# Performance work log

Measured on AMD Instinct MI355X. Metric: run time of the kernel, lower is better.

## Reference

```python
import jax, jax.numpy as jnp
import numpy as np

N_NODES = 50000
N_EDGES = 600000
HIDDEN = 128
HEADS = 8
OUT_CH = HIDDEN // HEADS
NUM_LAYERS = 3
NEG_SLOPE = 0.2   # PyG GATConv default leaky_relu slope
BN_EPS = 1e-5

# Note: dropout is a no-op in eval mode; BatchNorm uses batch statistics
# (training-mode math, the only well-defined choice without running stats).

def setup_inputs() -> dict:
    key = jax.random.key(0)
    ks = jax.random.split(key, 9)
    x = jax.random.normal(ks[0], (N_NODES, HIDDEN), dtype=jnp.float32)
    edge_index = jax.random.randint(ks[1], (2, N_EDGES), 0, N_NODES, dtype=jnp.int64)
    s = 1.0 / np.sqrt(HIDDEN)
    W = jax.random.normal(ks[2], (NUM_LAYERS, HIDDEN, HEADS * OUT_CH), dtype=jnp.float32) * s
    att_src = jax.random.normal(ks[3], (NUM_LAYERS, HEADS, OUT_CH), dtype=jnp.float32) * s
    att_dst = jax.random.normal(ks[4], (NUM_LAYERS, HEADS, OUT_CH), dtype=jnp.float32) * s
    bias = jnp.zeros((NUM_LAYERS, HIDDEN), dtype=jnp.float32)
    gamma = jnp.ones((NUM_LAYERS, HIDDEN), dtype=jnp.float32)
    beta = jnp.zeros((NUM_LAYERS, HIDDEN), dtype=jnp.float32)
    return {"x": x, "edge_index": edge_index, "W": W, "att_src": att_src,
            "att_dst": att_dst, "bias": bias, "gamma": gamma, "beta": beta}


def _gat_layer(x, src, dst, W, a_src, a_dst, b):
    n = x.shape[0]
    h = (x @ W).reshape(n, HEADS, OUT_CH)              # [N,H,C]
    alpha_s = jnp.einsum('nhc,hc->nh', h, a_src)        # [N,H]
    alpha_d = jnp.einsum('nhc,hc->nh', h, a_dst)
    e = jax.nn.leaky_relu(alpha_s[src] + alpha_d[dst], NEG_SLOPE)  # [E,H]
    # segment softmax over incoming edges of each destination node
    m = jax.ops.segment_max(e, dst, num_segments=n)     # [N,H]
    e = jnp.exp(e - m[dst])
    z = jax.ops.segment_sum(e, dst, num_segments=n)
    alpha = e / (z[dst] + 1e-16)                        # [E,H]
    msg = h[src] * alpha[:, :, None]                    # [E,H,C]
    out = jax.ops.segment_sum(msg, dst, num_segments=n) # [N,H,C]
    return out.reshape(n, HEADS * OUT_CH) + b


def _batchnorm(x, gamma, beta):
    mu = x.mean(axis=0)
    var = x.var(axis=0)
    return (x - mu) * jax.lax.rsqrt(var + BN_EPS) * gamma + beta


def reference(x, edge_index, W, att_src, att_dst, bias, gamma, beta):
    src, dst = edge_index[0], edge_index[1]
    for l in range(NUM_LAYERS):
        x = _gat_layer(x, src, dst, W[l], att_src[l], att_dst[l], bias[l])
        x = _batchnorm(x, gamma[l], beta[l])
        x = jax.nn.elu(x)
    return x
```

## Files before the change

### kernel.cpp

```cpp
#include <hip/hip_runtime.h>
#include <hip/hip_bf16.h>

#define N_NODES 50000
#define N_EDGES 600000
#define HID 128
#define HEADS 8
#define OUTC 16
#define NEG_SLOPE 0.2f
#define BN_EPS 1e-5f

typedef __attribute__((ext_vector_type(8))) short short8;
typedef __attribute__((ext_vector_type(4))) float floatx4;

__device__ __forceinline__ float bf_lo(unsigned int v) { return __uint_as_float(v << 16); }
__device__ __forceinline__ float bf_hi(unsigned int v) { return __uint_as_float(v & 0xffff0000u); }

__device__ __forceinline__ short f2bfs(float v) {
    __hip_bfloat16 b = __float2bfloat16(v);
    return *reinterpret_cast<short*>(&b);
}

__global__ void k_hist_prep(const int* __restrict__ dst, int* __restrict__ deg, int e, int nb_e,
                            const float* __restrict__ W, const float* __restrict__ asrc,
                            const float* __restrict__ adst,
                            __hip_bfloat16* __restrict__ Wt, __hip_bfloat16* __restrict__ WAT) {
    if ((int)blockIdx.x < nb_e) {
        int i = blockIdx.x * 256 + threadIdx.x;
        if (i < e) atomicAdd(&deg[dst[i]], 1);
        return;
    }
    int i = (blockIdx.x - nb_e) * 256 + threadIdx.x;
    if (i < 3 * 16384) {
        int l = i >> 14, r = i & 16383, n = r >> 7, k = r & 127;
        Wt[i] = __float2bfloat16(W[l * 16384 + k * 128 + n]);
    } else {
        int j2 = i - 3 * 16384;
        if (j2 < 3 * 2048) {
            int l = j2 >> 11, r = j2 & 2047, j = r >> 7, k = r & 127;
            const float* att = (j < 8) ? (asrc + l * 128 + j * 16) : (adst + l * 128 + (j - 8) * 16);
            const float* Wrow = W + l * 16384 + k * 128 + (j & 7) * 16;
            float sum = 0.f;
#pragma unroll
            for (int c = 0; c < 16; c++) sum += Wrow[c] * att[c];
            WAT[j2] = __float2bfloat16(sum);
        }
    }
}

__global__ void k_scan1(const int* __restrict__ deg, int* __restrict__ incl,
                        int* __restrict__ partials, int n) {
    __shared__ int sh[512];
    int i = blockIdx.x * 512 + threadIdx.x;
    int v = (i < n) ? deg[i] : 0;
    sh[threadIdx.x] = v;
    __syncthreads();
    for (int off = 1; off < 512; off <<= 1) {
        int t = (threadIdx.x >= off) ? sh[threadIdx.x - off] : 0;
        __syncthreads();
        sh[threadIdx.x] += t;
        __syncthreads();
    }
    if (i < n) incl[i] = sh[threadIdx.x];
    if (threadIdx.x == 511) partials[blockIdx.x] = sh[511];
}

__global__ void k_scan2(int* __restrict__ partials, int nb) {
    __shared__ int sh[128];
    int v = (threadIdx.x < nb) ? partials[threadIdx.x] : 0;
    sh[threadIdx.x] = v;
    __syncthreads();
    for (int off = 1; off < 128; off <<= 1) {
        int t = (threadIdx.x >= off) ? sh[threadIdx.x - off] : 0;
        __syncthreads();
        sh[threadIdx.x] += t;
        __syncthreads();
    }
    if (threadIdx.x < nb) partials[threadIdx.x] = sh[threadIdx.x] - v;
}

__global__ void k_scan3(const int* __restrict__ deg, const int* __restrict__ incl,
                        const int* __restrict__ partials, int* __restrict__ row_ptr,
                        int* __restrict__ cursor, int n, int e_total) {
    int i = blockIdx.x * 512 + threadIdx.x;
    if (i < n) {
        int rp = incl[i] - deg[i] + partials[blockIdx.x];
        row_ptr[i] = rp;
        cursor[i] = rp;
    }
    if (i == 0) row_ptr[n] = e_total;
}

__global__ void k_scatter(const int* __restrict__ src, const int* __restrict__ dst,
                          int* __restrict__ cursor, int* __restrict__ col_src, int e) {
    int i = blockIdx.x * 256 + threadIdx.x;
    if (i < e) {
        int d = dst[i];
        int p = atomicAdd(&cursor[d], 1);
        col_src[p] = src[i];
    }
}

__global__ __launch_bounds__(256) void k_gemm(const float* __restrict__ Xf,
                                              const float* __restrict__ stats,
                                              const float* __restrict__ gamma,
                                              const float* __restrict__ beta,
                                              const __hip_bfloat16* __restrict__ Wt,
                                              const __hip_bfloat16* __restrict__ WAT,
                                              __hip_bfloat16* __restrict__ Hb,
                                              float* __restrict__ AS, float* __restrict__ AD,
                                              int n_nodes, int apply_bn) {
    __shared__ float s_scale[128], s_shift[128];
    if (apply_bn && threadIdx.x < 128) {
        int c = threadIdx.x;
        float invN = 1.0f / (float)N_NODES;
        float mu = stats[c] * invN;
        float var = stats[128 + c] * invN - mu * mu;
        float sc = rsqrtf(var + BN_EPS) * gamma[c];
        s_scale[c] = sc;
        s_shift[c] = beta[c] - mu * sc;
    }
    __syncthreads();

    int wave = threadIdx.x >> 6, lane = threadIdx.x & 63;
    int row0 = blockIdx.x * 64 + wave * 16;
    int m_lane = lane & 15, kq = lane >> 4;
    floatx4 acc[8] = {};
    floatx4 acc_a = {};
    const short* Ws = (const short*)Wt;
    const short* Was = (const short*)WAT;
    int r = row0 + m_lane;
    int rr = (r < n_nodes) ? r : 0;
    for (int c = 0; c < 4; c++) {
        const float4* xp = (const float4*)(Xf + (size_t)rr * 128 + c * 32 + kq * 8);
        float4 v0 = xp[0], v1 = xp[1];
        float vals[8] = {v0.x, v0.y, v0.z, v0.w, v1.x, v1.y, v1.z, v1.w};
        short8 a;
        if (apply_bn) {
            int ch0 = c * 32 + kq * 8;
#pragma unroll
            for (int j = 0; j < 8; j++) {
                float val = fmaf(vals[j], s_scale[ch0 + j], s_shift[ch0 + j]);
                val = (val > 0.f) ? val : (__expf(val) - 1.0f);
                a[j] = f2bfs(val);
            }
        } else {
#pragma unroll
            for (int j = 0; j < 8; j++)
                a[j] = f2bfs(vals[j]);
        }
        for (int t = 0; t < 8; t++) {
            short8 b = *(const short8*)(Ws + (t * 16 + m_lane) * 128 + c * 32 + kq * 8);
            acc[t] = __builtin_amdgcn_mfma_f32_16x16x32_bf16(a, b, acc[t], 0, 0, 0);
        }
        short8 bwa = *(const short8*)(Was + m_lane * 128 + c * 32 + kq * 8);
        acc_a = __builtin_amdgcn_mfma_f32_16x16x32_bf16(a, bwa, acc_a, 0, 0, 0);
    }
#pragma unroll
    for (int reg = 0; reg < 4; reg++) {
        int row = row0 + kq * 4 + reg;
        if (row >= n_nodes) continue;
#pragma unroll
        for (int t = 0; t < 8; t++)
            Hb[(size_t)row * 128 + t * 16 + m_lane] = __float2bfloat16(acc[t][reg]);
        float av = acc_a[reg];
        if (m_lane < 8) AS[row * 8 + m_lane] = av;
        else            AD[row * 8 + (m_lane - 8)] = av;
    }
}

__global__ __launch_bounds__(256) void k_agg(const int* __restrict__ RP,
                                             const int* __restrict__ COL,
                                             const float* __restrict__ AS,
                                             const float* __restrict__ AD,
                                             const __hip_bfloat16* __restrict__ Hb,
                                             const float* __restrict__ bias,
                                             float* __restrict__ out, int n_nodes) {
    int wave = threadIdx.x >> 6, lane = threadIdx.x & 63;
    int n = blockIdx.x * 4 + wave;
    if (n >= n_nodes) return;
    int e_l = lane >> 4, q = lane & 15, h = q >> 1;
    int p0 = RP[n], p1 = RP[n + 1];
    float ad = AD[n * 8 + h];
    float z = 0.f;
    float acc[8];
#pragma unroll
    for (int c = 0; c < 8; c++) acc[c] = 0.f;
    const unsigned short* Hu = (const unsigned short*)Hb;
    for (int p = p0 + e_l; p < p1; p += 4) {
        int s = COL[p];
        float e = AS[s * 8 + h] + ad;
        e = (e > 0.f) ? e : NEG_SLOPE * e;
        float w = __expf(e);
        z += w;
        const uint4 hv = *(const uint4*)(Hu + (size_t)s * 128 + q * 8);
        acc[0] += w * bf_lo(hv.x); acc[1] += w * bf_hi(hv.x);
        acc[2] += w * bf_lo(hv.y); acc[3] += w * bf_hi(hv.y);
        acc[4] += w * bf_lo(hv.z); acc[5] += w * bf_hi(hv.z);
        acc[6] += w * bf_lo(hv.w); acc[7] += w * bf_hi(hv.w);
    }
#pragma unroll
    for (int off = 16; off < 64; off <<= 1) {
        z += __shfl_xor(z, off, 64);
#pragma unroll
        for (int c = 0; c < 8; c++) acc[c] += __shfl_xor(acc[c], off, 64);
    }
    if (e_l == 0) {
        float inv = 1.0f / (z + 1e-16f);
        const float* bp = bias + q * 8;
        float4* op = (float4*)(out + (size_t)n * 128 + q * 8);
        op[0] = make_float4(fmaf(acc[0], inv, bp[0]), fmaf(acc[1], inv, bp[1]),
                            fmaf(acc[2], inv, bp[2]), fmaf(acc[3], inv, bp[3]));
        op[1] = make_float4(fmaf(acc[4], inv, bp[4]), fmaf(acc[5], inv, bp[5]),
                            fmaf(acc[6], inv, bp[6]), fmaf(acc[7], inv, bp[7]));
    }
}

__global__ __launch_bounds__(256) void k_bnstats(const float* __restrict__ x,
                                                 float* __restrict__ partials, int n_nodes) {
    int tid = threadIdx.x;
    int c4 = tid & 31, sub = tid >> 5;
    int g = blockIdx.x * 8 + sub;
    float sx = 0.f, sy = 0.f, sz = 0.f, sw = 0.f;
    float qx = 0.f, qy = 0.f, qz = 0.f, qw = 0.f;
    for (int n = g; n < n_nodes; n += 2048) {
        float4 v = *(const float4*)(x + (size_t)n * 128 + c4 * 4);
        sx += v.x; sy += v.y; sz += v.z; sw += v.w;
        qx += v.x * v.x; qy += v.y * v.y; qz += v.z * v.z; qw += v.w * v.w;
    }
    __shared__ float ssum[8][128];
    __shared__ float ssq[8][128];
    int c = c4 * 4;
    ssum[sub][c] = sx; ssum[sub][c + 1] = sy; ssum[sub][c + 2] = sz; ssum[sub][c + 3] = sw;
    ssq[sub][c] = qx;  ssq[sub][c + 1] = qy;  ssq[sub][c + 2] = qz;  ssq[sub][c + 3] = qw;
    __syncthreads();
    float total = 0.f;
    if (tid < 128) {
#pragma unroll
        for (int k = 0; k < 8; k++) total += ssum[k][tid];
    } else {
        int cc = tid - 128;
#pragma unroll
        for (int k = 0; k < 8; k++) total += ssq[k][cc];
    }
    partials[blockIdx.x * 256 + tid] = total;
}

__global__ void k_bnreduce(const float* __restrict__ partials, float* __restrict__ stats) {
    int t = threadIdx.x;
    float s = 0.f;
#pragma unroll 8
    for (int b = 0; b < 256; b++) s += partials[b * 256 + t];
    stats[t] = s;
}

__global__ void k_bnapply(const float* __restrict__ x, const float* __restrict__ stats,
                          const float* __restrict__ gamma, const float* __restrict__ beta,
                          float* __restrict__ outf, int n_nodes) {
    int i = blockIdx.x * 256 + threadIdx.x;
    if (i >= n_nodes * 32) return;
    float4 v = *(const float4*)(x + (size_t)i * 4);
    int c0 = (i * 4) & 127;
    float r[4] = {v.x, v.y, v.z, v.w};
    float invN = 1.0f / (float)N_NODES;
#pragma unroll
    for (int j = 0; j < 4; j++) {
        int c = c0 + j;
        float mu = stats[c] * invN;
        float var = stats[128 + c] * invN - mu * mu;
        float sc = rsqrtf(var + BN_EPS) * gamma[c];
        float val = (r[j] - mu) * sc + beta[c];
        val = (val > 0.f) ? val : (__expf(val) - 1.0f);
        r[j] = val;
    }
    *(float4*)(outf + (size_t)i * 4) = make_float4(r[0], r[1], r[2], r[3]);
}

extern "C" void kernel_launch(void* const* d_in, const int* in_sizes, int n_in,
                              void* d_out, int out_size, void* d_ws, size_t ws_size,
                              hipStream_t stream) {
    const float* x_in   = (const float*)d_in[0];
    const int*   eidx   = (const int*)d_in[1];
    const float* W      = (const float*)d_in[2];
    const float* attsrc = (const float*)d_in[3];
    const float* attdst = (const float*)d_in[4];
    const float* bias   = (const float*)d_in[5];
    const float* gamma  = (const float*)d_in[6];
    const float* beta   = (const float*)d_in[7];
    float* out = (float*)d_out;

    const int N = N_NODES, E = N_EDGES;
    const int* src = eidx;
    const int* dst = eidx + E;

    char* base = (char*)d_ws;
    size_t off = 0;
    auto carve = [&](size_t bytes) -> char* {
        char* p = base + off;
        off += (bytes + 255) & ~(size_t)255;
        return p;
    };
    __hip_bfloat16* Hb  = (__hip_bfloat16*)carve((size_t)N * HID * 2);
    float*          XN  = (float*)carve((size_t)N * HID * 4);
    float*          AS  = (float*)carve((size_t)N * HEADS * 4);
    float*          AD  = (float*)carve((size_t)N * HEADS * 4);
    __hip_bfloat16* WT  = (__hip_bfloat16*)carve((size_t)3 * HID * HID * 2);
    __hip_bfloat16* WAT = (__hip_bfloat16*)carve((size_t)3 * 16 * HID * 2);
    float*          STA = (float*)carve(3 * 256 * 4);
    float*          PAR = (float*)carve(256 * 256 * 4);
    int*            DEG = (int*)carve((size_t)N * 4);
    int*            INC = (int*)carve((size_t)N * 4);
    int*            RP  = (int*)carve((size_t)(N + 1) * 4);
    int*            CUR = (int*)carve((size_t)N * 4);
    int*            PRT = (int*)carve(1024 * 4);
    int*            COL = (int*)carve((size_t)E * 4);

    const int NB_E  = (E + 255) / 256;
    const int NB_SC = (N + 511) / 512;
    const int PREP_B = (3 * 16384 + 3 * 2048 + 255) / 256;

    (void)hipMemsetAsync(DEG, 0, (size_t)N * 4, stream);

    k_hist_prep<<<NB_E + PREP_B, 256, 0, stream>>>(dst, DEG, E, NB_E, W, attsrc, attdst, WT, WAT);
    k_scan1<<<NB_SC, 512, 0, stream>>>(DEG, INC, PRT, N);
    k_scan2<<<1, 128, 0, stream>>>(PRT, NB_SC);
    k_scan3<<<NB_SC, 512, 0, stream>>>(DEG, INC, PRT, RP, CUR, N, E);
    k_scatter<<<NB_E, 256, 0, stream>>>(src, dst, CUR, COL, E);

    for (int l = 0; l < 3; l++) {
        const float* Xf = (l == 0) ? x_in : XN;
        const float* st = (l == 0) ? nullptr : (STA + (l - 1) * 256);
        const float* gm = gamma + (l - 1) * 128;
        const float* bt = beta + (l - 1) * 128;
        k_gemm<<<(N + 63) / 64, 256, 0, stream>>>(Xf, st, gm, bt,
                                                  WT + l * 16384, WAT + l * 2048,
                                                  Hb, AS, AD, N, (l == 0) ? 0 : 1);
        k_agg<<<(N + 3) / 4, 256, 0, stream>>>(RP, COL, AS, AD, Hb, bias + l * 128, XN, N);
        k_bnstats<<<256, 256, 0, stream>>>(XN, PAR, N);
        k_bnreduce<<<1, 256, 0, stream>>>(PAR, STA + l * 256);
    }
    k_bnapply<<<(N * 32 + 255) / 256, 256, 0, stream>>>(XN, STA + 2 * 256,
                                                        gamma + 2 * 128, beta + 2 * 128, out, N);
}
```

Baseline: 387.5 us.

## Fuse BatchNorm statistics accumulation into aggregation kernel via atomics

The aggregation kernel now also reduces per-channel sum and sum-of-squares for its four nodes in shared memory and atomically adds them into 64 striped partial buffers. This removes the separate bnstats kernel, which re-read the full 50000x128 fp32 output. The reduce kernel sums the 64 stripes and zeroes them for the next layer, and the initial memset is widened to clear the buffer. The cost is 256 atomics per block across 12500 blocks, contention on the stripes, and an early exit replaced by a block-wide barrier.

Measured after the change: 364.8 us. 1.06x faster.

```diff
diff --git a/kernel.cpp b/kernel.cpp
--- a/kernel.cpp
+++ b/kernel.cpp
@@ -174,13 +174,20 @@
                                              const float* __restrict__ AD,
                                              const __hip_bfloat16* __restrict__ Hb,
                                              const float* __restrict__ bias,
-                                             float* __restrict__ out, int n_nodes) {
+                                             float* __restrict__ out,
+                                             float* __restrict__ par2, int n_nodes) {
+    __shared__ float s_sum[4][128];
+    __shared__ float s_sq[4][128];
     int wave = threadIdx.x >> 6, lane = threadIdx.x & 63;
     int n = blockIdx.x * 4 + wave;
-    if (n >= n_nodes) return;
+    bool valid = (n < n_nodes);
     int e_l = lane >> 4, q = lane & 15, h = q >> 1;
-    int p0 = RP[n], p1 = RP[n + 1];
-    float ad = AD[n * 8 + h];
+    s_sum[wave][lane] = 0.f; s_sum[wave][lane + 64] = 0.f;
+    s_sq[wave][lane] = 0.f;  s_sq[wave][lane + 64] = 0.f;
+
+    int p0 = valid ? RP[n] : 0;
+    int p1 = valid ? RP[n + 1] : 0;
+    float ad = valid ? AD[n * 8 + h] : 0.f;
     float z = 0.f;
     float acc[8];
 #pragma unroll
@@ -204,53 +211,42 @@
 #pragma unroll
         for (int c = 0; c < 8; c++) acc[c] += __shfl_xor(acc[c], off, 64);
     }
-    if (e_l == 0) {
+    if (valid && e_l == 0) {
         float inv = 1.0f / (z + 1e-16f);
         const float* bp = bias + q * 8;
+        float v[8];
+#pragma unroll
+        for (int c = 0; c < 8; c++) v[c] = fmaf(acc[c], inv, bp[c]);
         float4* op = (float4*)(out + (size_t)n * 128 + q * 8);
-        op[0] = make_float4(fmaf(acc[0], inv, bp[0]), fmaf(acc[1], inv, bp[1]),
-                            fmaf(acc[2], inv, bp[2]), fmaf(acc[3], inv, bp[3]));
-        op[1] = make_float4(fmaf(acc[4], inv, bp[4]), fmaf(acc[5], inv, bp[5]),
-                            fmaf(acc[6], inv, bp[6]), fmaf(acc[7], inv, bp[7]));
-    }
-}
-
-__global__ __launch_bounds__(256) void k_bnstats(const float* __restrict__ x,
-                                                 float* __restrict__ partials, int n_nodes) {
+        op[0] = make_float4(v[0], v[1], v[2], v[3]);
+        op[1] = make_float4(v[4], v[5], v[6], v[7]);
+        int ch0 = q * 8;
+#pragma unroll
+        for (int c = 0; c < 8; c++) {
+            s_sum[wave][ch0 + c] = v[c];
+            s_sq[wave][ch0 + c] = v[c] * v[c];
+        }
+    }
+    __syncthreads();
     int tid = threadIdx.x;
-    int c4 = tid & 31, sub = tid >> 5;
-    int g = blockIdx.x * 8 + sub;
-    float sx = 0.f, sy = 0.f, sz = 0.f, sw = 0.f;
-    float qx = 0.f, qy = 0.f, qz = 0.f, qw = 0.f;
-    for (int n = g; n < n_nodes; n += 2048) {
-        float4 v = *(const float4*)(x + (size_t)n * 128 + c4 * 4);
-        sx += v.x; sy += v.y; sz += v.z; sw += v.w;
-        qx += v.x * v.x; qy += v.y * v.y; qz += v.z * v.z; qw += v.w * v.w;
-    }
-    __shared__ float ssum[8][128];
-    __shared__ float ssq[8][128];
-    int c = c4 * 4;
-    ssum[sub][c] = sx; ssum[sub][c + 1] = sy; ssum[sub][c + 2] = sz; ssum[sub][c + 3] = sw;
-    ssq[sub][c] = qx;  ssq[sub][c + 1] = qy;  ssq[sub][c + 2] = qz;  ssq[sub][c + 3] = qw;
-    __syncthreads();
-    float total = 0.f;
+    float tot;
     if (tid < 128) {
-#pragma unroll
-        for (int k = 0; k < 8; k++) total += ssum[k][tid];
+        tot = s_sum[0][tid] + s_sum[1][tid] + s_sum[2][tid] + s_sum[3][tid];
     } else {
         int cc = tid - 128;
-#pragma unroll
-        for (int k = 0; k < 8; k++) total += ssq[k][cc];
-    }
-    partials[blockIdx.x * 256 + tid] = total;
-}
-
-__global__ void k_bnreduce(const float* __restrict__ partials, float* __restrict__ stats) {
+        tot = s_sq[0][cc] + s_sq[1][cc] + s_sq[2][cc] + s_sq[3][cc];
+    }
+    atomicAdd(&par2[(blockIdx.x & 63) * 256 + tid], tot);
+}
+
+__global__ void k_bnreduce(float* __restrict__ par2, float* __restrict__ stats) {
     int t = threadIdx.x;
     float s = 0.f;
 #pragma unroll 8
-    for (int b = 0; b < 256; b++) s += partials[b * 256 + t];
+    for (int b = 0; b < 64; b++) s += par2[b * 256 + t];
     stats[t] = s;
+#pragma unroll 8
+    for (int b = 0; b < 64; b++) par2[b * 256 + t] = 0.f;
 }
 
 __global__ void k_bnapply(const float* __restrict__ x, const float* __restrict__ stats,
@@ -306,8 +302,8 @@
     __hip_bfloat16* WT  = (__hip_bfloat16*)carve((size_t)3 * HID * HID * 2);
     __hip_bfloat16* WAT = (__hip_bfloat16*)carve((size_t)3 * 16 * HID * 2);
     float*          STA = (float*)carve(3 * 256 * 4);
-    float*          PAR = (float*)carve(256 * 256 * 4);
     int*            DEG = (int*)carve((size_t)N * 4);
+    float*          PAR2 = (float*)carve(64 * 256 * 4);
     int*            INC = (int*)carve((size_t)N * 4);
     int*            RP  = (int*)carve((size_t)(N + 1) * 4);
     int*            CUR = (int*)carve((size_t)N * 4);
@@ -318,7 +314,8 @@
     const int NB_SC = (N + 511) / 512;
     const int PREP_B = (3 * 16384 + 3 * 2048 + 255) / 256;
 
-    (void)hipMemsetAsync(DEG, 0, (size_t)N * 4, stream);
+    size_t zlen = (size_t)((char*)(PAR2 + 64 * 256) - (char*)DEG);
+    (void)hipMemsetAsync(DEG, 0, zlen, stream);
 
     k_hist_prep<<<NB_E + PREP_B, 256, 0, stream>>>(dst, DEG, E, NB_E, W, attsrc, attdst, WT, WAT);
     k_scan1<<<NB_SC, 512, 0, stream>>>(DEG, INC, PRT, N);
@@ -334,9 +331,9 @@
         k_gemm<<<(N + 63) / 64, 256, 0, stream>>>(Xf, st, gm, bt,
                                                   WT + l * 16384, WAT + l * 2048,
                                                   Hb, AS, AD, N, (l == 0) ? 0 : 1);
-        k_agg<<<(N + 3) / 4, 256, 0, stream>>>(RP, COL, AS, AD, Hb, bias + l * 128, XN, N);
-        k_bnstats<<<256, 256, 0, stream>>>(XN, PAR, N);
-        k_bnreduce<<<1, 256, 0, stream>>>(PAR, STA + l * 256);
+        k_agg<<<(N + 3) / 4, 256, 0, stream>>>(RP, COL, AS, AD, Hb, bias + l * 128,
+                                               XN, PAR2, N);
+        k_bnreduce<<<1, 256, 0, stream>>>(PAR2, STA + l * 256);
     }
     k_bnapply<<<(N * 32 + 255) / 256, 256, 0, stream>>>(XN, STA + 2 * 256,
                                                         gamma + 2 * 128, beta + 2 * 128, out, N);
```
